# Kernel optimization log

Measured on AMD Instinct MI355X. Metric: run time of the kernel, lower is better.

The kernel has to match this reference:

```python
import jax, jax.numpy as jnp
import numpy as np

N = 100000
E = 3200000
IN_DIM, HID, MLP_HID, K = 3, 64, 128, 15


def setup_inputs() -> dict:
    key = jax.random.key(0)
    ks = jax.random.split(key, 10)
    x = jax.random.normal(ks[0], (N, IN_DIM), dtype=jnp.float32)
    edge_index = jax.random.randint(ks[1], (2, E), 0, N, dtype=jnp.int32)
    def glorot(k, shape):
        lim = float(np.sqrt(6.0 / (shape[0] + shape[1])))
        return jax.random.uniform(k, shape, jnp.float32, -lim, lim)
    return {
        "x": x,
        "edge_index": edge_index,
        "W1": glorot(ks[2], (IN_DIM, HID)), "b1": jnp.zeros((HID,), jnp.float32),
        "W2": glorot(ks[3], (HID, HID)),    "b2": jnp.zeros((HID,), jnp.float32),
        "Wm1": glorot(ks[4], (HID, MLP_HID)), "bm1": jnp.zeros((MLP_HID,), jnp.float32),
        "Wm2": glorot(ks[5], (MLP_HID, K)),   "bm2": jnp.zeros((K,), jnp.float32),
    }


def _gcn_layer(h, W, b, src, dst, deg_inv_sqrt, n):
    # h: [N, Fin] -> [N, Fout]; GCNConv: D^-1/2 (A+I) D^-1/2 (h W) + b
    hw = h @ W  # dense GEMM first (Fin small)
    norm = deg_inv_sqrt[src] * deg_inv_sqrt[dst]  # [E+N]
    msg = hw[src] * norm[:, None]                 # irregular gather, [E+N, Fout]
    out = jax.ops.segment_sum(msg, dst, num_segments=n)  # scatter-add
    return out + b


def reference(x, edge_index, W1, b1, W2, b2, Wm1, bm1, Wm2, bm2):
    n = x.shape[0]
    loops = jnp.arange(n, dtype=edge_index.dtype)
    src = jnp.concatenate([edge_index[0], loops])  # self-loops appended
    dst = jnp.concatenate([edge_index[1], loops])
    deg = jax.ops.segment_sum(jnp.ones_like(dst, dtype=x.dtype), dst, num_segments=n)
    deg_inv_sqrt = jnp.where(deg > 0, jax.lax.rsqrt(jnp.maximum(deg, 1.0)), 0.0)

    h = jax.nn.elu(_gcn_layer(x, W1, b1, src, dst, deg_inv_sqrt, n))
    h = jax.nn.elu(_gcn_layer(h, W2, b2, src, dst, deg_inv_sqrt, n))
    # MLP (dropout is identity in eval mode)
    h = jax.nn.elu(h @ Wm1 + bm1)
    H = h @ Wm2 + bm2
    return jax.nn.softmax(H, axis=1)  # [N, K]
```

## Files before the change

kernel.cpp:

```cpp
#include <hip/hip_runtime.h>
#include <hip/hip_fp16.h>
#include <math.h>


#define SPAN 128
#define CAP  4608
#define CH   8192
#define EPT  16
#define H2P  88
#define MSP2 136

typedef _Float16 v8hf __attribute__((ext_vector_type(8)));
typedef float    v4f  __attribute__((ext_vector_type(4)));

__device__ __forceinline__ float elu(float v) { return v > 0.f ? v : expm1f(v); }

__global__ __launch_bounds__(512) void scatter_kernel(const int* __restrict__ src,
    const int* __restrict__ dst, int* __restrict__ cursor, unsigned* __restrict__ colb,
    const float* __restrict__ W2, const float* __restrict__ Wm1,
    const float* __restrict__ Wm2, __half* __restrict__ W2t,
    __half* __restrict__ Wm1t, __half* __restrict__ Wm2p,
    int E, int NBK, int nChunks) {
    int tid = threadIdx.x;
    if ((int)blockIdx.x == nChunks) {
        for (int i = tid; i < 64 * 64; i += 512) {
            int f = i >> 6, k = i & 63;
            W2t[f * 64 + k] = __float2half(W2[k * 64 + f]);
        }
        for (int i = tid; i < 128 * 64; i += 512) {
            int j = i >> 6, f = i & 63;
            Wm1t[j * 64 + f] = __float2half(Wm1[f * 128 + j]);
        }
        for (int i = tid; i < 4 * 64 * 8; i += 512) {
            int j = i & 7, l = (i >> 3) & 63, t = i >> 9;
            int k = t * 32 + (l >> 4) * 8 + j;
            int c = l & 15;
            Wm2p[i] = (c < 15) ? __float2half(Wm2[k * 15 + c]) : __half(0.f);
        }
        return;
    }
    __shared__ int hist[1024];
    __shared__ unsigned gb[1024];
    int chunk = blockIdx.x;
    for (int i = tid; i < NBK; i += 512) hist[i] = 0;
    __syncthreads();
    int base = chunk * CH;
    int cnt = min(CH, E - base);
    unsigned br[EPT], dt[EPT];
#pragma unroll
    for (int j = 0; j < EPT; ++j) {
        int idx = j * 512 + tid;
        br[j] = 0xFFFFFFFFu;
        if (idx < cnt) {
            int e = base + idx;
            int s = src[e], d = dst[e];
            int b = d >> 7;
            int r = atomicAdd(&hist[b], 1);
            br[j] = ((unsigned)b << 13) | (unsigned)r;
            dt[j] = ((unsigned)(d & 127) << 17) | (unsigned)s;
        }
    }
    __syncthreads();
    for (int b = tid; b < NBK; b += 512) {
        int c = hist[b];
        gb[b] = (unsigned)(b * CAP) + (c ? (unsigned)atomicAdd(&cursor[b], c) : 0u);
    }
    __syncthreads();
#pragma unroll
    for (int j = 0; j < EPT; ++j) {
        if (br[j] != 0xFFFFFFFFu) {
            int b = br[j] >> 13;
            int r = br[j] & 8191;
            unsigned pos = gb[b] + (unsigned)r;
            if (pos < (unsigned)(b + 1) * CAP) colb[pos] = dt[j];
        }
    }
}

__global__ __launch_bounds__(512) void csr_sort_kernel(unsigned* __restrict__ colb,
    const int* __restrict__ cursor, const float* __restrict__ x,
    uint2* __restrict__ rp2, float* __restrict__ dis, __half* __restrict__ sxh,
    int N) {
    __shared__ __align__(16) unsigned ebuf[CAP];
    __shared__ __align__(16) int sbuf[CAP];
    __shared__ int cnt[SPAN], pref[SPAN], fill[SPAN];
    int b = blockIdx.x, tid = threadIdx.x;
    int n = min(cursor[b], CAP);
    size_t base = (size_t)b * CAP;
    if (tid < SPAN) cnt[tid] = 0;
    int n4 = n >> 2;
    for (int k = tid; k < n4; k += 512)
        *(uint4*)(ebuf + 4 * k) = *(const uint4*)(colb + base + 4 * k);
    for (int i = (n4 << 2) + tid; i < n; i += 512) ebuf[i] = colb[base + i];
    __syncthreads();
    for (int i = tid; i < n; i += 512) atomicAdd(&cnt[(ebuf[i] >> 17) & 127], 1);
    __syncthreads();
    if (tid < SPAN) pref[tid] = cnt[tid];
    __syncthreads();
    for (int off = 1; off < SPAN; off <<= 1) {
        int xv = (tid < SPAN && tid >= off) ? pref[tid - off] : 0;
        __syncthreads();
        if (tid < SPAN) pref[tid] += xv;
        __syncthreads();
    }
    if (tid < SPAN) {
        int ex = pref[tid] - cnt[tid];
        fill[tid] = ex;
        int node = b * SPAN + tid;
        if (node < N) {
            uint2 rp;
            rp.x = (unsigned)(base + ex);
            rp.y = (unsigned)(base + ex + cnt[tid]);
            rp2[node] = rp;
            float r = rsqrtf((float)(cnt[tid] + 1));
            dis[node] = r;
            __half2 h0 = __floats2half2_rn(r * x[node * 3 + 0], r * x[node * 3 + 1]);
            __half2 h1 = __floats2half2_rn(r * x[node * 3 + 2], 0.f);
            uint2 w; w.x = *(unsigned*)&h0; w.y = *(unsigned*)&h1;
            *(uint2*)(sxh + (size_t)node * 4) = w;
        }
    }
    __syncthreads();
    for (int i = tid; i < n; i += 512) {
        unsigned e = ebuf[i];
        int pos = atomicAdd(&fill[(e >> 17) & 127], 1);
        sbuf[pos] = (int)(e & 0x1FFFF);
    }
    __syncthreads();
    for (int k = tid; k < n4; k += 512)
        *(uint4*)(colb + base + 4 * k) = *(const uint4*)(sbuf + 4 * k);
    for (int i = (n4 << 2) + tid; i < n; i += 512) colb[base + i] = (unsigned)sbuf[i];
}

__global__ void agg3_kernel(const __half* __restrict__ sxh, const uint2* __restrict__ rp2,
                            const unsigned* __restrict__ colb, const float* __restrict__ dis,
                            const float* __restrict__ W1, const float* __restrict__ b1,
                            __half* __restrict__ s1h, int N) {
    int wave = (blockIdx.x * blockDim.x + threadIdx.x) >> 6;
    int lane = threadIdx.x & 63;
    int hl = lane & 31;
    int d = wave * 2 + (lane >> 5);
    bool act = d < N;
    int start = 0, end = 0;
    if (act) { uint2 rp = rp2[d]; start = (int)rp.x; end = (int)rp.y; }
    float a0 = 0.f, a1 = 0.f, a2v = 0.f;
    for (int i = start + hl; i < end; i += 32) {
        uint2 rq = *(const uint2*)(sxh + (size_t)colb[i] * 4);
        float2 u0 = __half22float2(*(__half2*)&rq.x);
        float2 u1 = __half22float2(*(__half2*)&rq.y);
        a0 += u0.x; a1 += u0.y; a2v += u1.x;
    }
#pragma unroll
    for (int off = 16; off; off >>= 1) {
        a0  += __shfl_xor(a0, off);
        a1  += __shfl_xor(a1, off);
        a2v += __shfl_xor(a2v, off);
    }
    if (act) {
        uint2 rq = *(const uint2*)(sxh + (size_t)d * 4);
        float2 u0 = __half22float2(*(__half2*)&rq.x);
        float2 u1 = __half22float2(*(__half2*)&rq.y);
        a0 += u0.x; a1 += u0.y; a2v += u1.x;
        float r = dis[d];
        float v0 = r * (a0 * W1[hl]      + a1 * W1[64 + hl]      + a2v * W1[128 + hl])      + b1[hl];
        float v1 = r * (a0 * W1[32 + hl] + a1 * W1[96 + hl]      + a2v * W1[160 + hl])      + b1[32 + hl];
        s1h[(size_t)d * 64 + hl]      = __float2half(r * elu(v0));
        s1h[(size_t)d * 64 + 32 + hl] = __float2half(r * elu(v1));
    }
}

__global__ void agg64_kernel(const __half* __restrict__ s1h, const uint2* __restrict__ rp2,
                             const unsigned* __restrict__ colb, const float* __restrict__ dis,
                             __half* __restrict__ a2h, int N) {
    int wave = (blockIdx.x * blockDim.x + threadIdx.x) >> 6;
    int lane = threadIdx.x & 63;
    int g = lane >> 3;
    int f = lane & 7;
    int d = wave;
    if (d >= N) return;
    uint2 rp = rp2[d];
    int start = (int)rp.x;
    int ne = (int)(rp.y - rp.x);
    int nslots = ne + 1;
    int npair = (nslots + 15) >> 4;
    float acc0 = 0.f, acc1 = 0.f, acc2 = 0.f, acc3 = 0.f;
    float acc4 = 0.f, acc5 = 0.f, acc6 = 0.f, acc7 = 0.f;
    for (int p = 0; p < npair; ++p) {
        int ja = p * 16 + g;
        int jb = ja + 8;
        int ca = (int)colb[start + ja];
        int cb = (int)colb[start + jb];
        bool oa = ja < nslots, ob = jb < nslots;
        ca = (ja < ne) ? ca : d;
        cb = (jb < ne) ? cb : d;
        uint4 A = *(const uint4*)(s1h + (size_t)ca * 64 + f * 8);
        uint4 B = *(const uint4*)(s1h + (size_t)cb * 64 + f * 8);
        A.x = oa ? A.x : 0u; A.y = oa ? A.y : 0u;
        A.z = oa ? A.z : 0u; A.w = oa ? A.w : 0u;
        B.x = ob ? B.x : 0u; B.y = ob ? B.y : 0u;
        B.z = ob ? B.z : 0u; B.w = ob ? B.w : 0u;
        __half2 p0 = __hadd2(*(__half2*)&A.x, *(__half2*)&B.x);
        __half2 p1 = __hadd2(*(__half2*)&A.y, *(__half2*)&B.y);
        __half2 p2 = __hadd2(*(__half2*)&A.z, *(__half2*)&B.z);
        __half2 p3 = __hadd2(*(__half2*)&A.w, *(__half2*)&B.w);
        float2 q0 = __half22float2(p0);
        float2 q1 = __half22float2(p1);
        float2 q2 = __half22float2(p2);
        float2 q3 = __half22float2(p3);
        acc0 += q0.x; acc1 += q0.y; acc2 += q1.x; acc3 += q1.y;
        acc4 += q2.x; acc5 += q2.y; acc6 += q3.x; acc7 += q3.y;
    }
#pragma unroll
    for (int off = 8; off <= 32; off <<= 1) {
        acc0 += __shfl_xor(acc0, off);
        acc1 += __shfl_xor(acc1, off);
        acc2 += __shfl_xor(acc2, off);
        acc3 += __shfl_xor(acc3, off);
        acc4 += __shfl_xor(acc4, off);
        acc5 += __shfl_xor(acc5, off);
        acc6 += __shfl_xor(acc6, off);
        acc7 += __shfl_xor(acc7, off);
    }
    float r = dis[d];
    if (g == 0) {
        __half2 o0 = __floats2half2_rn(r * acc0, r * acc1);
        __half2 o1 = __floats2half2_rn(r * acc2, r * acc3);
        __half2 o2 = __floats2half2_rn(r * acc4, r * acc5);
        __half2 o3 = __floats2half2_rn(r * acc6, r * acc7);
        uint4 w;
        w.x = *(unsigned*)&o0; w.y = *(unsigned*)&o1;
        w.z = *(unsigned*)&o2; w.w = *(unsigned*)&o3;
        *(uint4*)(a2h + (size_t)d * 64 + f * 8) = w;
    }
}

__global__ __launch_bounds__(256) void h1_kernel(const __half* __restrict__ a2h,
    const __half* __restrict__ W2t, const float* __restrict__ b2g,
    const __half* __restrict__ Wm1t, const float* __restrict__ bm1g,
    const __half* __restrict__ Wm2p, const float* __restrict__ bm2g,
    float* __restrict__ out, int N) {
    __shared__ __align__(16) __half h2s[64 * H2P];
    __shared__ __align__(16) __half ms[64 * MSP2];
    int tid = threadIdx.x;
    int wave = tid >> 6, lane = tid & 63;
    int q = lane >> 4, l16 = lane & 15;
    int base = blockIdx.x * 64;

    v8hf wc[4];
#pragma unroll
    for (int t = 0; t < 4; ++t)
        wc[t] = *(const v8hf*)(Wm2p + ((size_t)(t * 64 + lane)) * 8);
    float bbc = (l16 < 15) ? bm2g[l16] : 0.f;

    {
        int nodeRow = base + wave * 16 + l16;
        size_t arow = (size_t)min(nodeRow, N - 1) * 64;
        v8hf af0 = *(const v8hf*)(a2h + arow + q * 8);
        v8hf af1 = *(const v8hf*)(a2h + arow + 32 + q * 8);
#pragma unroll
        for (int fb = 0; fb < 4; ++fb) {
            float bb = b2g[fb * 16 + l16];
            v4f acc = {bb, bb, bb, bb};
            v8hf b0 = *(const v8hf*)(W2t + (fb * 16 + l16) * 64 + q * 8);
            v8hf b1 = *(const v8hf*)(W2t + (fb * 16 + l16) * 64 + 32 + q * 8);
            acc = __builtin_amdgcn_mfma_f32_16x16x32_f16(af0, b0, acc, 0, 0, 0);
            acc = __builtin_amdgcn_mfma_f32_16x16x32_f16(af1, b1, acc, 0, 0, 0);
#pragma unroll
            for (int r = 0; r < 4; ++r)
                h2s[(wave * 16 + q * 4 + r) * H2P + fb * 16 + l16] =
                    __float2half(elu(acc[r]));
        }
    }
    __syncthreads();
    {
        int arow = (wave * 16 + l16) * H2P;
        v8hf af0 = *(const v8hf*)(h2s + arow + q * 8);
        v8hf af1 = *(const v8hf*)(h2s + arow + 32 + q * 8);
#pragma unroll
        for (int jb = 0; jb < 8; ++jb) {
            float bb = bm1g[jb * 16 + l16];
            v4f acc = {bb, bb, bb, bb};
            v8hf b0 = *(const v8hf*)(Wm1t + (jb * 16 + l16) * 64 + q * 8);
            v8hf b1 = *(const v8hf*)(Wm1t + (jb * 16 + l16) * 64 + 32 + q * 8);
            acc = __builtin_amdgcn_mfma_f32_16x16x32_f16(af0, b0, acc, 0, 0, 0);
            acc = __builtin_amdgcn_mfma_f32_16x16x32_f16(af1, b1, acc, 0, 0, 0);
#pragma unroll
            for (int r = 0; r < 4; ++r)
                ms[(wave * 16 + q * 4 + r) * MSP2 + jb * 16 + l16] =
                    __float2half(elu(acc[r]));
        }
    }
    __syncthreads();
    {
        int arow = (wave * 16 + l16) * MSP2;
        v4f accC = {bbc, bbc, bbc, bbc};
#pragma unroll
        for (int t = 0; t < 4; ++t) {
            v8hf a = *(const v8hf*)(ms + arow + t * 32 + q * 8);
            accC = __builtin_amdgcn_mfma_f32_16x16x32_f16(a, wc[t], accC, 0, 0, 0);
        }
#pragma unroll
        for (int r = 0; r < 4; ++r) {
            float lg = (l16 < 15) ? accC[r] : -1e30f;
            float mx = lg;
            mx = fmaxf(mx, __shfl_xor(mx, 1));
            mx = fmaxf(mx, __shfl_xor(mx, 2));
            mx = fmaxf(mx, __shfl_xor(mx, 4));
            mx = fmaxf(mx, __shfl_xor(mx, 8));
            float ex = (l16 < 15) ? __expf(lg - mx) : 0.f;
            float sden = ex;
            sden += __shfl_xor(sden, 1);
            sden += __shfl_xor(sden, 2);
            sden += __shfl_xor(sden, 4);
            sden += __shfl_xor(sden, 8);
            int node = base + wave * 16 + q * 4 + r;
            if (l16 < 15 && node < N)
                out[(size_t)node * 15 + l16] = ex / sden;
        }
    }
}

extern "C" void kernel_launch(void* const* d_in, const int* in_sizes, int n_in,
                              void* d_out, int out_size, void* d_ws, size_t ws_size,
                              hipStream_t stream) {
    const float* x   = (const float*)d_in[0];
    const int*   ei  = (const int*)d_in[1];
    const float* W1  = (const float*)d_in[2];
    const float* b1  = (const float*)d_in[3];
    const float* W2  = (const float*)d_in[4];
    const float* b2  = (const float*)d_in[5];
    const float* Wm1 = (const float*)d_in[6];
    const float* bm1 = (const float*)d_in[7];
    const float* Wm2 = (const float*)d_in[8];
    const float* bm2 = (const float*)d_in[9];
    float* out = (float*)d_out;

    int N = in_sizes[0] / 3;
    int E = in_sizes[1] / 2;
    const int* src = ei;
    const int* dst = ei + E;
    int NBK = (N + SPAN - 1) / SPAN;

    uintptr_t p = (uintptr_t)d_ws;
    auto carve = [&](size_t bytes) -> void* {
        p = (p + 255) & ~(uintptr_t)255;
        void* r = (void*)p;
        p += bytes;
        return r;
    };
    unsigned* colb    = (unsigned*)carve((size_t)NBK * CAP * 4 + 256);
    __half*   a2h     = (__half*)carve((size_t)N * 64 * 2);
    __half*   s1h     = (__half*)carve((size_t)N * 64 * 2);
    int*      cursor  = (int*)carve((size_t)NBK * 4);
    uint2*    rp2     = (uint2*)carve((size_t)N * 8);
    float*    dis     = (float*)carve((size_t)N * 4);
    __half*   sxh     = (__half*)carve((size_t)N * 8);
    __half*   W2t     = (__half*)carve(64 * 64 * 2);
    __half*   Wm1t    = (__half*)carve(128 * 64 * 2);
    __half*   Wm2p    = (__half*)carve(4 * 64 * 8 * 2);

    int nChunks = (E + CH - 1) / CH;
    int aggBlocks = (N + 7) / 8;
    int aggBlocks64 = (N + 3) / 4;
    int nTiles = (N + 63) / 64;

    hipMemsetAsync(cursor, 0, (size_t)NBK * 4, stream);
    scatter_kernel<<<nChunks + 1, 512, 0, stream>>>(src, dst, cursor, colb,
        W2, Wm1, Wm2, W2t, Wm1t, Wm2p, E, NBK, nChunks);
    csr_sort_kernel<<<NBK, 512, 0, stream>>>(colb, cursor, x, rp2, dis, sxh, N);
    agg3_kernel<<<aggBlocks, 256, 0, stream>>>(sxh, rp2, colb, dis, W1, b1, s1h, N);
    agg64_kernel<<<aggBlocks64, 256, 0, stream>>>(s1h, rp2, colb, dis, a2h, N);
    h1_kernel<<<nTiles, 256, 0, stream>>>(a2h, W2t, b2, Wm1t, bm1, Wm2p, bm2, out, N);
}
```

Baseline: 233.0 us.

## Pad CSR rows to multiples of 16 with self-loop and zero sentinel node

```diff
diff --git a/kernel.cpp b/kernel.cpp
--- a/kernel.cpp
+++ b/kernel.cpp
@@ -4,7 +4,7 @@
 
 
 #define SPAN 128
-#define CAP  4608
+#define CAP  6400
 #define CH   8192
 #define EPT  16
 #define H2P  88
@@ -20,7 +20,8 @@
     const float* __restrict__ W2, const float* __restrict__ Wm1,
     const float* __restrict__ Wm2, __half* __restrict__ W2t,
     __half* __restrict__ Wm1t, __half* __restrict__ Wm2p,
-    int E, int NBK, int nChunks) {
+    __half* __restrict__ s1h, __half* __restrict__ sxh,
+    int E, int NBK, int nChunks, int N) {
     int tid = threadIdx.x;
     if ((int)blockIdx.x == nChunks) {
         for (int i = tid; i < 64 * 64; i += 512) {
@@ -36,6 +37,10 @@
             int k = t * 32 + (l >> 4) * 8 + j;
             int c = l & 15;
             Wm2p[i] = (c < 15) ? __float2half(Wm2[k * 15 + c]) : __half(0.f);
+        }
+        if (tid < 32) {
+            ((uint2*)(s1h + (size_t)N * 64))[tid & 15] = uint2{0u, 0u};
+            if (tid == 16) *((uint2*)(sxh + (size_t)N * 4)) = uint2{0u, 0u};
         }
         return;
     }
@@ -95,7 +100,12 @@
     __syncthreads();
     for (int i = tid; i < n; i += 512) atomicAdd(&cnt[(ebuf[i] >> 17) & 127], 1);
     __syncthreads();
-    if (tid < SPAN) pref[tid] = cnt[tid];
+    int myPk = 0;
+    if (tid < SPAN) {
+        int node = b * SPAN + tid;
+        myPk = (node < N) ? ((cnt[tid] + 1 + 15) & ~15) : 0;
+        pref[tid] = myPk;
+    }
     __syncthreads();
     for (int off = 1; off < SPAN; off <<= 1) {
         int xv = (tid < SPAN && tid >= off) ? pref[tid - off] : 0;
@@ -103,21 +113,25 @@
         if (tid < SPAN) pref[tid] += xv;
         __syncthreads();
     }
+    int ntot = pref[SPAN - 1];
     if (tid < SPAN) {
-        int ex = pref[tid] - cnt[tid];
-        fill[tid] = ex;
+        int offP = pref[tid] - myPk;
+        fill[tid] = offP;
         int node = b * SPAN + tid;
         if (node < N) {
+            int c = cnt[tid];
             uint2 rp;
-            rp.x = (unsigned)(base + ex);
-            rp.y = (unsigned)(base + ex + cnt[tid]);
+            rp.x = (unsigned)(base + offP);
+            rp.y = (unsigned)(base + offP + myPk);
             rp2[node] = rp;
-            float r = rsqrtf((float)(cnt[tid] + 1));
+            float r = rsqrtf((float)(c + 1));
             dis[node] = r;
             __half2 h0 = __floats2half2_rn(r * x[node * 3 + 0], r * x[node * 3 + 1]);
             __half2 h1 = __floats2half2_rn(r * x[node * 3 + 2], 0.f);
             uint2 w; w.x = *(unsigned*)&h0; w.y = *(unsigned*)&h1;
             *(uint2*)(sxh + (size_t)node * 4) = w;
+            sbuf[offP + c] = node;
+            for (int j = c + 1; j < myPk; ++j) sbuf[offP + j] = N;
         }
     }
     __syncthreads();
@@ -127,9 +141,9 @@
         sbuf[pos] = (int)(e & 0x1FFFF);
     }
     __syncthreads();
-    for (int k = tid; k < n4; k += 512)
+    int nt4 = (ntot + 3) >> 2;
+    for (int k = tid; k < nt4; k += 512)
         *(uint4*)(colb + base + 4 * k) = *(const uint4*)(sbuf + 4 * k);
-    for (int i = (n4 << 2) + tid; i < n; i += 512) colb[base + i] = (unsigned)sbuf[i];
 }
 
 __global__ void agg3_kernel(const __half* __restrict__ sxh, const uint2* __restrict__ rp2,
@@ -157,10 +171,6 @@
         a2v += __shfl_xor(a2v, off);
     }
     if (act) {
-        uint2 rq = *(const uint2*)(sxh + (size_t)d * 4);
-        float2 u0 = __half22float2(*(__half2*)&rq.x);
-        float2 u1 = __half22float2(*(__half2*)&rq.y);
-        a0 += u0.x; a1 += u0.y; a2v += u1.x;
         float r = dis[d];
         float v0 = r * (a0 * W1[hl]      + a1 * W1[64 + hl]      + a2v * W1[128 + hl])      + b1[hl];
         float v1 = r * (a0 * W1[32 + hl] + a1 * W1[96 + hl]      + a2v * W1[160 + hl])      + b1[32 + hl];
@@ -179,26 +189,14 @@
     int d = wave;
     if (d >= N) return;
     uint2 rp = rp2[d];
-    int start = (int)rp.x;
-    int ne = (int)(rp.y - rp.x);
-    int nslots = ne + 1;
-    int npair = (nslots + 15) >> 4;
+    int i = (int)rp.x, end = (int)rp.y;
     float acc0 = 0.f, acc1 = 0.f, acc2 = 0.f, acc3 = 0.f;
     float acc4 = 0.f, acc5 = 0.f, acc6 = 0.f, acc7 = 0.f;
-    for (int p = 0; p < npair; ++p) {
-        int ja = p * 16 + g;
-        int jb = ja + 8;
-        int ca = (int)colb[start + ja];
-        int cb = (int)colb[start + jb];
-        bool oa = ja < nslots, ob = jb < nslots;
-        ca = (ja < ne) ? ca : d;
-        cb = (jb < ne) ? cb : d;
+    for (; i < end; i += 16) {
+        int ca = (int)colb[i + g];
+        int cb = (int)colb[i + 8 + g];
         uint4 A = *(const uint4*)(s1h + (size_t)ca * 64 + f * 8);
         uint4 B = *(const uint4*)(s1h + (size_t)cb * 64 + f * 8);
-        A.x = oa ? A.x : 0u; A.y = oa ? A.y : 0u;
-        A.z = oa ? A.z : 0u; A.w = oa ? A.w : 0u;
-        B.x = ob ? B.x : 0u; B.y = ob ? B.y : 0u;
-        B.z = ob ? B.z : 0u; B.w = ob ? B.w : 0u;
         __half2 p0 = __hadd2(*(__half2*)&A.x, *(__half2*)&B.x);
         __half2 p1 = __hadd2(*(__half2*)&A.y, *(__half2*)&B.y);
         __half2 p2 = __hadd2(*(__half2*)&A.z, *(__half2*)&B.z);
@@ -350,11 +348,11 @@
     };
     unsigned* colb    = (unsigned*)carve((size_t)NBK * CAP * 4 + 256);
     __half*   a2h     = (__half*)carve((size_t)N * 64 * 2);
-    __half*   s1h     = (__half*)carve((size_t)N * 64 * 2);
+    __half*   s1h     = (__half*)carve((size_t)(N + 1) * 64 * 2);
     int*      cursor  = (int*)carve((size_t)NBK * 4);
     uint2*    rp2     = (uint2*)carve((size_t)N * 8);
     float*    dis     = (float*)carve((size_t)N * 4);
-    __half*   sxh     = (__half*)carve((size_t)N * 8);
+    __half*   sxh     = (__half*)carve((size_t)(N + 1) * 8);
     __half*   W2t     = (__half*)carve(64 * 64 * 2);
     __half*   Wm1t    = (__half*)carve(128 * 64 * 2);
     __half*   Wm2p    = (__half*)carve(4 * 64 * 8 * 2);
@@ -366,7 +364,7 @@
 
     hipMemsetAsync(cursor, 0, (size_t)NBK * 4, stream);
     scatter_kernel<<<nChunks + 1, 512, 0, stream>>>(src, dst, cursor, colb,
-        W2, Wm1, Wm2, W2t, Wm1t, Wm2p, E, NBK, nChunks);
+        W2, Wm1, Wm2, W2t, Wm1t, Wm2p, s1h, sxh, E, NBK, nChunks, N);
     csr_sort_kernel<<<NBK, 512, 0, stream>>>(colb, cursor, x, rp2, dis, sxh, N);
     agg3_kernel<<<aggBlocks, 256, 0, stream>>>(sxh, rp2, colb, dis, W1, b1, s1h, N);
     agg64_kernel<<<aggBlocks64, 256, 0, stream>>>(s1h, rp2, colb, dis, a2h, N);
```

After: 236.6 us. About the same (+1.5%).
